# Performance work log

Measured on AMD Instinct MI355X. Metric: run time of the kernel, lower is better.

Reference implementation:

```python
import jax, jax.numpy as jnp
import numpy as np

B, T, H, W = 2, 8, 14, 14
S = H * W
DIM, HEADS = 768, 12
HD = DIM // HEADS  # 64


def setup_inputs() -> dict:
    key = jax.random.key(0)
    ks = jax.random.split(key, 6)
    std = 0.02
    return {
        "x": jax.random.normal(ks[0], (B, T, S, DIM), jnp.float32),
        "qkv_w": jax.random.normal(ks[1], (3 * DIM, DIM), jnp.float32) * std,
        "proj_w": jax.random.normal(ks[2], (DIM, DIM), jnp.float32) * std,
        "proj_b": jnp.zeros((DIM,), jnp.float32),
        "rel_pos_h": jax.random.normal(ks[3], (2 * H - 1, HD), jnp.float32) * std,
        "rel_pos_w": jax.random.normal(ks[4], (2 * W - 1, HD), jnp.float32) * std,
        "rel_pos_t": jax.random.normal(ks[5], (2 * T - 1, HD), jnp.float32) * std,
    }


def _rel_table(rel_pos, q_len):
    # q_len == k_len here, so get_rel_pos is identity and indices simplify
    idx = np.arange(q_len)[:, None] - np.arange(q_len)[None, :] + (q_len - 1)
    return rel_pos[idx]  # [q_len, k_len, head_dim]


def reference(x, qkv_w, proj_w, proj_b, rel_pos_h, rel_pos_w, rel_pos_t):
    B_, T_, S_, C = x.shape
    H_ = W_ = int(S_ ** 0.5)
    N = T_ * S_
    hd = C // HEADS
    scale = hd ** -0.5

    xf = x.reshape(B_, N, C)
    qkv = (xf @ qkv_w.T).reshape(B_, N, 3, HEADS, hd).transpose(2, 0, 3, 1, 4)
    q, k, v = qkv[0], qkv[1], qkv[2]  # each [B, heads, N, hd]

    attn = jnp.einsum('bhqd,bhkd->bhqk', q, k) * scale  # [B, heads, N, N]

    # Decomposed relative-position bias (note: uses UNscaled q, as in original)
    r_q = q.reshape(B_, HEADS, T_, H_, W_, hd)
    Rh = _rel_table(rel_pos_h, H_)  # [H, H, hd]
    Rw = _rel_table(rel_pos_w, W_)  # [W, W, hd]
    Rt = _rel_table(rel_pos_t, T_)  # [T, T, hd]
    rel_h = jnp.einsum('bythwc,hkc->bythwk', r_q, Rh)
    rel_w = jnp.einsum('bythwc,wkc->bythwk', r_q, Rw)
    rel_t = jnp.einsum('bythwc,tkc->bythwk', r_q, Rt)

    attn = (attn.reshape(B_, HEADS, T_, H_, W_, T_, H_, W_)
            + rel_h[:, :, :, :, :, None, :, None]
            + rel_w[:, :, :, :, :, None, None, :]
            + rel_t[:, :, :, :, :, :, None, None]
            ).reshape(B_, HEADS, N, N)

    attn = jax.nn.softmax(attn, axis=-1)
    out = jnp.einsum('bhqk,bhkd->bhqd', attn, v)  # [B, heads, N, hd]
    out = out.transpose(0, 2, 1, 3).reshape(B_, N, C)
    out = out @ proj_w.T + proj_b
    return out.reshape(B_, T_, S_, C)
```

## Files before the change

### kernel.cpp

```cpp
#include <hip/hip_runtime.h>

using f16   = _Float16;
using f16x4 = __attribute__((ext_vector_type(4))) _Float16;
using f16x8 = __attribute__((ext_vector_type(8))) _Float16;
using f32x4 = __attribute__((ext_vector_type(4))) float;
using u32x4 = __attribute__((ext_vector_type(4))) unsigned int;
using fp16x2_raw = __fp16 __attribute__((ext_vector_type(2)));

#define MFMA16(a, b, c) __builtin_amdgcn_mfma_f32_16x16x32_f16((a), (b), (c), 0, 0, 0)

namespace {
constexpr int kT = 8, kWd = 14, kS = 196;
constexpr int kN = 1568;
constexpr int kM = 3136;
constexpr int kHeads = 12;
constexpr int kNp = 1664;
constexpr float kLog2e = 1.4426950408889634f;
constexpr size_t OFF_WH   = 0;
constexpr size_t OFF_WP   = 3538944;
constexpr size_t OFF_Q    = 4718592;
constexpr size_t OFF_XH   = 9830400;
constexpr size_t OFF_KF   = 14942208;
constexpr size_t OFF_KONE = 20054016;
constexpr size_t OFF_VSWZ = 20267008;
constexpr size_t WS_TOTAL = 25378816;
constexpr int kKoneTot = 13 * 8 * 2 * 64 * 8;

__device__ inline f16x4 pack4(float4 v) {
  union { fp16x2_raw h2[2]; f16x4 f4; } u;
  u.h2[0] = __builtin_amdgcn_cvt_pkrtz(v.x, v.y);
  u.h2[1] = __builtin_amdgcn_cvt_pkrtz(v.z, v.w);
  return u.f4;
}

__device__ inline float fast_exp2(float x) {
#if __has_builtin(__builtin_amdgcn_exp2f)
  return __builtin_amdgcn_exp2f(x);
#else
  return __expf(x * 0.6931471805599453f);
#endif
}

__device__ inline void gload_lds16(const f16* g, f16* l) {
  __builtin_amdgcn_global_load_lds(
      (const __attribute__((address_space(1))) unsigned int*)g,
      (__attribute__((address_space(3))) unsigned int*)l,
      16, 0, 0);
}

__device__ inline float dotqLDS(const f16x8* qh, const f16* Rrow) {
  float s = 0.f;
#pragma unroll
  for (int i = 0; i < 8; ++i) {
    f16x8 a = qh[i];
    f16x8 b = *(const f16x8*)(Rrow + i * 8);
#pragma unroll
    for (int k = 0; k < 8; ++k) s += (float)a[k] * (float)b[k];
  }
  return s;
}
}

__global__ __launch_bounds__(256) void arp_cvt(
    const float* __restrict__ qkvw, const float* __restrict__ projw,
    const float* __restrict__ X,
    f16* __restrict__ Wh, f16* __restrict__ Wp, f16* __restrict__ Xh,
    f16* __restrict__ konefrag) {
  int gid = blockIdx.x * 256 + threadIdx.x;
  const int NQ = (2304 * 768) / 4;
  const int NP = (768 * 768) / 4;
  const int NX = (3136 * 768) / 4;
  if (gid < NQ) {
    *(f16x4*)(Wh + (size_t)gid * 4) = pack4(*(const float4*)(qkvw + (size_t)gid * 4));
  } else if (gid < NQ + NP) {
    int g = gid - NQ;
    *(f16x4*)(Wp + (size_t)g * 4) = pack4(*(const float4*)(projw + (size_t)g * 4));
  } else if (gid < NQ + NP + NX) {
    int g = gid - NQ - NP;
    *(f16x4*)(Xh + (size_t)g * 4) = pack4(*(const float4*)(X + (size_t)g * 4));
  } else {
    int g = gid - NQ - NP - NX;
    if (g < kKoneTot) {
      int j = g & 7;
      int lane = (g >> 3) & 63;
      int s2 = (g >> 9) & 1;
      int nt = (g >> 10) & 7;
      int kt = g >> 13;
      int slot = lane & 15, qd = lane >> 4;
      int kin = (nt >> 1) * 32 + (slot >> 2) * 8 + (nt & 1) * 4 + (slot & 3);
      int key = kt * 128 + kin;
      int c = s2 * 32 + qd * 8 + j;
      int t2 = key / kS; int rm = key - t2 * kS;
      int h2 = rm / kWd; int w2 = rm - h2 * kWd;
      if (t2 > kT - 1) t2 = kT - 1;
      float v = 0.f;
      if (c == h2) v = 1.f;
      else if (c == 14 + w2) v = 1.f;
      else if (c == 28 + t2) v = 1.f;
      else if (c == 36 && key >= kN) v = 1.f;
      konefrag[g] = (f16)v;
    }
  }
}

__global__ __launch_bounds__(256, 2) void arp_gemm_qkv(
    const f16* __restrict__ Xh, const f16* __restrict__ Wh,
    f16* __restrict__ qf, f16* __restrict__ kfrag, f16* __restrict__ vswz) {
  __shared__ char smem[34816];
  f16* sA = (f16*)smem;
  f16* sB = (f16*)(smem + 10240);
  f16* sE = (f16*)smem;
  const int tid = threadIdx.x, lane = tid & 63, wv = tid >> 6;
  const int m0 = blockIdx.y * 128, n0 = blockIdx.x * 128;
  const int wm = (wv & 1) * 64, wn = (wv >> 1) * 64;
  const int frow = lane & 15, quad = lane >> 4, fcol = quad * 8;
  const f32x4 vzero = {0.f, 0.f, 0.f, 0.f};
  f32x4 acc[4][4];
#pragma unroll
  for (int i = 0; i < 4; ++i)
#pragma unroll
    for (int j = 0; j < 4; ++j) acc[i][j] = vzero;

  u32x4 pA[2], pB[2];
  const u32x4 uz = {0, 0, 0, 0};
#pragma unroll
  for (int i = 0; i < 2; ++i) {
    int idx = i * 256 + tid;
    int r = idx >> 2, c8 = (idx & 3) * 8;
    int gm = m0 + r;
    pA[i] = (gm < kM) ? *(const u32x4*)(Xh + (size_t)gm * 768 + c8) : uz;
    pB[i] = *(const u32x4*)(Wh + (size_t)(n0 + r) * 768 + c8);
  }

  for (int kt = 0; kt < 24; ++kt) {
#pragma unroll
    for (int i = 0; i < 2; ++i) {
      int idx = i * 256 + tid;
      int r = idx >> 2, c8 = (idx & 3) * 8;
      *(u32x4*)&sA[r * 40 + c8] = pA[i];
      *(u32x4*)&sB[r * 40 + c8] = pB[i];
    }
    __syncthreads();
    if (kt < 23) {
      int ko = (kt + 1) * 32;
#pragma unroll
      for (int i = 0; i < 2; ++i) {
        int idx = i * 256 + tid;
        int r = idx >> 2, c8 = (idx & 3) * 8;
        int gm = m0 + r;
        pA[i] = (gm < kM) ? *(const u32x4*)(Xh + (size_t)gm * 768 + ko + c8) : uz;
        pB[i] = *(const u32x4*)(Wh + (size_t)(n0 + r) * 768 + ko + c8);
      }
    }
    f16x8 af[4], bf[4];
#pragma unroll
    for (int t = 0; t < 4; ++t) {
      af[t] = *(const f16x8*)&sA[(wm + t * 16 + frow) * 40 + fcol];
      bf[t] = *(const f16x8*)&sB[(wn + t * 16 + frow) * 40 + fcol];
    }
#pragma unroll
    for (int mt = 0; mt < 4; ++mt)
#pragma unroll
      for (int nt = 0; nt < 4; ++nt)
        acc[mt][nt] = MFMA16(af[mt], bf[nt], acc[mt][nt]);
    __syncthreads();
  }

  const int which = n0 / 768;
  if (which == 2) {
#pragma unroll
    for (int mt = 0; mt < 4; ++mt)
#pragma unroll
      for (int nt = 0; nt < 4; ++nt) {
        int cl = wn + nt * 16 + frow;
#pragma unroll
        for (int rg = 0; rg < 4; ++rg) {
          int rl = wm + mt * 16 + quad * 4 + rg;
          sE[cl * 136 + rl] = (f16)acc[mt][nt][rg];
        }
      }
    __syncthreads();
    int cl = tid >> 1;
    int rb = (tid & 1) * 64;
    int rem = n0 + cl - 1536;
    int hh = rem >> 6, d = rem & 63;
    int td = d >> 4, fr = d & 15;
#pragma unroll
    for (int j = 0; j < 8; ++j) {
      int ms = m0 + rb + j * 8;
      if (ms < kM) {
        int bb = (ms >= kN) ? 1 : 0;
        int ns = ms - bb * kN;
        int bh = bb * kHeads + hh;
        int kt2 = ns >> 7, kr = ns & 127;
        int kc = kr >> 5, qd = (kr >> 3) & 3;
        f16* dst = vswz + ((((size_t)(bh * 13 + kt2)) * 4 + td) * 4 + kc) * 512
                        + (qd * 16 + fr) * 8;
        *(u32x4*)dst = *(const u32x4*)&sE[cl * 136 + rb + j * 8];
      }
    }
  } else {
#pragma unroll
    for (int mt = 0; mt < 4; ++mt) {
      int rbase = m0 + wm + mt * 16 + quad * 4;
#pragma unroll
      for (int nt = 0; nt < 4; ++nt) {
        int col0 = n0 + wn + nt * 16;
        int rem = col0 - which * 768;
        int hh = rem >> 6;
        int d = (rem & 63) + frow;
        int s = d >> 5, qd2 = (d >> 3) & 3, j = d & 7;
#pragma unroll
        for (int rg = 0; rg < 4; ++rg) {
          int m = rbase + rg;
          if (m < kM) {
            int bb = (m >= kN) ? 1 : 0;
            int ns = m - bb * kN;
            int bh = bb * kHeads + hh;
            float av = acc[mt][nt][rg];
            if (which == 0) {
              av *= kLog2e;
              qf[((size_t)bh * kNp + ns) * 64 + d] = (f16)av;
            } else {
              av *= 0.125f;
              int kt2 = ns >> 7;
              int kin = ns & 127;
              int nt2 = ((kin >> 5) << 1) | ((kin >> 2) & 1);
              int slot = ((kin >> 3) & 3) * 4 + (kin & 3);
              kfrag[(((size_t)(bh * 13 + kt2) * 8 + nt2) * 2 + s) * 512
                    + (qd2 * 16 + slot) * 8 + j] = (f16)av;
            }
          }
        }
      }
    }
  }
}

__global__ __launch_bounds__(256, 3) void arp_attn(
    const f16* qf,
    const float* __restrict__ Rh, const float* __restrict__ Rw, const float* __restrict__ Rt,
    const f16* __restrict__ kfrag, const f16* __restrict__ konefrag,
    const f16* __restrict__ vswz, f16* qfO) {
  __shared__ char pool[49152];
  f16* sKa = (f16*)pool;
  f16* sKb = (f16*)(pool + 16384);
  f16* sV  = (f16*)(pool + 32768);
  f16* sQE = (f16*)pool;
  f16* sR  = (f16*)(pool + 8192);

  const int tid = threadIdx.x, lane = tid & 63, wv = tid >> 6;
  const int q0 = blockIdx.x * 64;
  const int bh = blockIdx.y;
  const int frow = lane & 15, quad = lane >> 4;
  const f32x4 vzero = {0.f, 0.f, 0.f, 0.f};

  const f16* kba = kfrag + (size_t)bh * 13 * 8192;
  const f16* vba = vswz + (size_t)bh * 13 * 8192;

  for (int g = tid; g < 69 * 16; g += 256) {
    int row = g >> 4, c4 = (g & 15) * 4;
    const float* src = (row < 27) ? Rh + row * 64 + c4
                     : (row < 54) ? Rw + (row - 27) * 64 + c4
                                  : Rt + (row - 54) * 64 + c4;
    *(f16x4*)&sR[row * 72 + c4] = pack4(*(const float4*)src);
  }
  __syncthreads();

  {
    int q = q0 + lane;
    int qc = (q < kN) ? q : kN - 1;
    int tq = qc / kS, sr = qc - tq * kS;
    int hq = sr / kWd, wq = sr - hq * kWd;
    if (wv < 3) {
      f16x8 qh[8];
      const f16x8* qv8 = (const f16x8*)(qf + ((size_t)bh * kNp + q) * 64);
#pragma unroll
      for (int i = 0; i < 8; ++i) qh[i] = qv8[i];
      if (wv == 0) {
#pragma unroll
        for (int e = 0; e < 14; ++e)
          sQE[lane * 64 + e] = (f16)dotqLDS(qh, &sR[(hq - e + 13) * 72]);
      } else if (wv == 1) {
#pragma unroll
        for (int e = 0; e < 14; ++e)
          sQE[lane * 64 + 14 + e] = (f16)dotqLDS(qh, &sR[(wq - e + 40) * 72]);
      } else {
#pragma unroll
        for (int e = 0; e < 8; ++e)
          sQE[lane * 64 + 28 + e] = (f16)dotqLDS(qh, &sR[(tq - e + 61) * 72]);
      }
    } else {
      sQE[lane * 64 + 36] = (f16)(-30000.f);
#pragma unroll
      for (int e = 37; e < 64; ++e) sQE[lane * 64 + e] = (f16)0.f;
    }
  }
  __syncthreads();

  f16x8 aQ0, aQ1, aQE0, aQE1;
  {
    int row = q0 + wv * 16 + frow;
    const f16* qp = qf + ((size_t)bh * kNp + row) * 64;
    aQ0 = *(const f16x8*)(qp + quad * 8);
    aQ1 = *(const f16x8*)(qp + 32 + quad * 8);
    int rl = wv * 16 + frow;
    aQE0 = *(const f16x8*)&sQE[rl * 64 + quad * 8];
    aQE1 = *(const f16x8*)&sQE[rl * 64 + 32 + quad * 8];
  }
  __syncthreads();

#pragma unroll
  for (int i = 0; i < 4; ++i) {
    int u = (i * 256 + tid) * 8;
    gload_lds16(kba + u, sKa + u);
    gload_lds16(konefrag + u, sKb + u);
    gload_lds16(vba + u, sV + u);
  }

  float den = 0.f;
  f32x4 Oc[4];
#pragma unroll
  for (int t = 0; t < 4; ++t) Oc[t] = vzero;

  for (int kt = 0; kt < 13; ++kt) {
    __syncthreads();

    f32x4 Sc[8];
    __builtin_amdgcn_s_setprio(1);
#pragma unroll
    for (int nt = 0; nt < 8; ++nt) {
      const f16* ka = &sKa[nt * 1024 + lane * 8];
      const f16* kb = &sKb[nt * 1024 + lane * 8];
      f32x4 s = MFMA16(*(const f16x8*)(ka), aQ0, vzero);
      s = MFMA16(*(const f16x8*)(ka + 512), aQ1, s);
      s = MFMA16(*(const f16x8*)(kb), aQE0, s);
      Sc[nt] = MFMA16(*(const f16x8*)(kb + 512), aQE1, s);
    }
    __builtin_amdgcn_s_setprio(0);
    f16x8 bV[4][4];
#pragma unroll
    for (int td = 0; td < 4; ++td)
#pragma unroll
      for (int kc = 0; kc < 4; ++kc)
        bV[td][kc] = *(const f16x8*)&sV[(td * 4 + kc) * 512 + lane * 8];
    __syncthreads();

    if (kt < 12) {
      const f16* kfa = kba + (size_t)(kt + 1) * 8192;
      const f16* koa = konefrag + (size_t)(kt + 1) * 8192;
      const f16* vfa = vba + (size_t)(kt + 1) * 8192;
#pragma unroll
      for (int i = 0; i < 4; ++i) {
        int u = (i * 256 + tid) * 8;
        gload_lds16(kfa + u, sKa + u);
        gload_lds16(koa + u, sKb + u);
        gload_lds16(vfa + u, sV + u);
      }
    }

#pragma unroll
    for (int nt = 0; nt < 8; ++nt)
#pragma unroll
      for (int r = 0; r < 4; ++r)
        Sc[nt][r] = fast_exp2(Sc[nt][r]);

    __builtin_amdgcn_s_setprio(1);
#pragma unroll
    for (int kc = 0; kc < 4; ++kc) {
      union { _Float16 h[8]; f16x8 v; } up;
#pragma unroll
      for (int r = 0; r < 4; ++r) {
        up.h[r]     = (f16)Sc[2 * kc][r];
        up.h[4 + r] = (f16)Sc[2 * kc + 1][r];
      }
#pragma unroll
      for (int r = 0; r < 4; ++r)
        den += (float)up.h[r] + (float)up.h[4 + r];
#pragma unroll
      for (int td = 0; td < 4; ++td)
        Oc[td] = MFMA16(up.v, bV[td][kc], Oc[td]);
    }
    __builtin_amdgcn_s_setprio(0);
  }

  den += __shfl_xor(den, 16, 64);
  den += __shfl_xor(den, 32, 64);
  float lr[4];
#pragma unroll
  for (int r = 0; r < 4; ++r)
    lr[r] = 1.f / __shfl(den, quad * 4 + r, 64);
#pragma unroll
  for (int td = 0; td < 4; ++td)
#pragma unroll
    for (int r = 0; r < 4; ++r) {
      int row = q0 + wv * 16 + quad * 4 + r;
      if (row < kN) {
        float val = Oc[td][r] * lr[r];
        qfO[((size_t)bh * kNp + row) * 64 + td * 16 + frow] = (f16)val;
      }
    }
}

__global__ __launch_bounds__(256, 4) void arp_gemm_proj(
    const f16* A, const f16* __restrict__ Wp,
    const float* __restrict__ bias, float* __restrict__ out) {
  __shared__ f16 sA[64 * 40];
  __shared__ f16 sB[128 * 40];
  const int tid = threadIdx.x, lane = tid & 63, wv = tid >> 6;
  const int m0 = blockIdx.y * 64, n0 = blockIdx.x * 128;
  const int frow = lane & 15, quad = lane >> 4, fcol = quad * 8;
  const f32x4 vzero = {0.f, 0.f, 0.f, 0.f};
  f32x4 acc[8];
#pragma unroll
  for (int j = 0; j < 8; ++j) acc[j] = vzero;

  u32x4 pA, pB[2];
  {
    int r = tid >> 2, c8 = (tid & 3) * 8;
    int m = m0 + r;
    int bb = (m >= kN) ? 1 : 0;
    int ns = m - bb * kN;
    pA = *(const u32x4*)(A + ((size_t)(bb * kHeads) * kNp + ns) * 64 + c8);
#pragma unroll
    for (int i = 0; i < 2; ++i) {
      int idx = i * 256 + tid;
      int rb2 = idx >> 2, cb8 = (idx & 3) * 8;
      pB[i] = *(const u32x4*)(Wp + (size_t)(n0 + rb2) * 768 + cb8);
    }
  }

  for (int kt = 0; kt < 24; ++kt) {
    {
      int r = tid >> 2, c8 = (tid & 3) * 8;
      *(u32x4*)&sA[r * 40 + c8] = pA;
#pragma unroll
      for (int i = 0; i < 2; ++i) {
        int idx = i * 256 + tid;
        int rb2 = idx >> 2, cb8 = (idx & 3) * 8;
        *(u32x4*)&sB[rb2 * 40 + cb8] = pB[i];
      }
    }
    __syncthreads();
    if (kt < 23) {
      int k1 = kt + 1;
      int hd = k1 >> 1, dof = (k1 & 1) * 32;
      int r = tid >> 2, c8 = (tid & 3) * 8;
      int m = m0 + r;
      int bb = (m >= kN) ? 1 : 0;
      int ns = m - bb * kN;
      pA = *(const u32x4*)(A + ((size_t)(bb * kHeads + hd) * kNp + ns) * 64 + dof + c8);
#pragma unroll
      for (int i = 0; i < 2; ++i) {
        int idx = i * 256 + tid;
        int rb2 = idx >> 2, cb8 = (idx & 3) * 8;
        pB[i] = *(const u32x4*)(Wp + (size_t)(n0 + rb2) * 768 + k1 * 32 + cb8);
      }
    }
    f16x8 af = *(const f16x8*)&sA[(wv * 16 + frow) * 40 + fcol];
    f16x8 bf[8];
#pragma unroll
    for (int u = 0; u < 8; ++u)
      bf[u] = *(const f16x8*)&sB[(u * 16 + frow) * 40 + fcol];
#pragma unroll
    for (int u = 0; u < 8; ++u)
      acc[u] = MFMA16(af, bf[u], acc[u]);
    __syncthreads();
  }
#pragma unroll
  for (int u = 0; u < 8; ++u) {
    int col = n0 + u * 16 + frow;
    float bv = bias[col];
#pragma unroll
    for (int rg = 0; rg < 4; ++rg) {
      int m = m0 + wv * 16 + quad * 4 + rg;
      out[(size_t)m * 768 + col] = acc[u][rg] + bv;
    }
  }
}

extern "C" void kernel_launch(void* const* d_in, const int* in_sizes, int n_in,
                              void* d_out, int out_size, void* d_ws, size_t ws_size,
                              hipStream_t stream) {
  if (ws_size < WS_TOTAL) return;
  const float* x      = (const float*)d_in[0];
  const float* qkv_w  = (const float*)d_in[1];
  const float* proj_w = (const float*)d_in[2];
  const float* proj_b = (const float*)d_in[3];
  const float* rph    = (const float*)d_in[4];
  const float* rpw    = (const float*)d_in[5];
  const float* rpt    = (const float*)d_in[6];
  char* ws = (char*)d_ws;
  f16* Wh       = (f16*)(ws + OFF_WH);
  f16* Wp       = (f16*)(ws + OFF_WP);
  f16* qf       = (f16*)(ws + OFF_Q);
  f16* Xh       = (f16*)(ws + OFF_XH);
  f16* kfrag    = (f16*)(ws + OFF_KF);
  f16* konefrag = (f16*)(ws + OFF_KONE);
  f16* vswz     = (f16*)(ws + OFF_VSWZ);

  const int cvtTot = (2304 * 768 + 768 * 768 + 3136 * 768) / 4 + kKoneTot;
  arp_cvt<<<(cvtTot + 255) / 256, 256, 0, stream>>>(qkv_w, proj_w, x, Wh, Wp, Xh, konefrag);
  arp_gemm_qkv<<<dim3(18, 25), 256, 0, stream>>>(Xh, Wh, qf, kfrag, vswz);
  arp_attn<<<dim3(25, 24), 256, 0, stream>>>(qf, rph, rpw, rpt, kfrag, konefrag, vswz, qf);
  arp_gemm_proj<<<dim3(6, 49), 256, 0, stream>>>(qf, Wp, proj_b, (float*)d_out);
}
```

Before: 173.0 us.

## Split attention key tiles across two wave groups with LDS reduction

The attention block grows from 256 to 512 threads. Each pair of waves shares a 16-row query fragment, and each wave handles half of the 128 keys in every key tile. The partial outputs and denominators from the second half are summed through shared memory at the end. This doubles the waves available per block to hide latency and halves per-wave register use. The cost is an extra LDS reduction and synchronisation, and possibly fewer resident blocks per CU.

```diff
diff --git a/kernel.cpp b/kernel.cpp
--- a/kernel.cpp
+++ b/kernel.cpp
@@ -237,7 +237,7 @@
   }
 }
 
-__global__ __launch_bounds__(256, 3) void arp_attn(
+__global__ __launch_bounds__(512, 6) void arp_attn(
     const f16* qf,
     const float* __restrict__ Rh, const float* __restrict__ Rw, const float* __restrict__ Rt,
     const f16* __restrict__ kfrag, const f16* __restrict__ konefrag,
@@ -253,12 +253,14 @@
   const int q0 = blockIdx.x * 64;
   const int bh = blockIdx.y;
   const int frow = lane & 15, quad = lane >> 4;
+  const int rf = wv & 3;
+  const int kh = wv >> 2;
   const f32x4 vzero = {0.f, 0.f, 0.f, 0.f};
 
   const f16* kba = kfrag + (size_t)bh * 13 * 8192;
   const f16* vba = vswz + (size_t)bh * 13 * 8192;
 
-  for (int g = tid; g < 69 * 16; g += 256) {
+  for (int g = tid; g < 69 * 16; g += 512) {
     int row = g >> 4, c4 = (g & 15) * 4;
     const float* src = (row < 27) ? Rh + row * 64 + c4
                      : (row < 54) ? Rw + (row - 27) * 64 + c4
@@ -290,7 +292,7 @@
         for (int e = 0; e < 8; ++e)
           sQE[lane * 64 + 28 + e] = (f16)dotqLDS(qh, &sR[(tq - e + 61) * 72]);
       }
-    } else {
+    } else if (wv == 3) {
       sQE[lane * 64 + 36] = (f16)(-30000.f);
 #pragma unroll
       for (int e = 37; e < 64; ++e) sQE[lane * 64 + e] = (f16)0.f;
@@ -300,22 +302,21 @@
 
   f16x8 aQ0, aQ1, aQE0, aQE1;
   {
-    int row = q0 + wv * 16 + frow;
+    int row = q0 + rf * 16 + frow;
     const f16* qp = qf + ((size_t)bh * kNp + row) * 64;
     aQ0 = *(const f16x8*)(qp + quad * 8);
     aQ1 = *(const f16x8*)(qp + 32 + quad * 8);
-    int rl = wv * 16 + frow;
+    int rl = rf * 16 + frow;
     aQE0 = *(const f16x8*)&sQE[rl * 64 + quad * 8];
     aQE1 = *(const f16x8*)&sQE[rl * 64 + 32 + quad * 8];
   }
   __syncthreads();
 
-#pragma unroll
-  for (int i = 0; i < 4; ++i) {
-    int u = (i * 256 + tid) * 8;
-    gload_lds16(kba + u, sKa + u);
-    gload_lds16(konefrag + u, sKb + u);
-    gload_lds16(vba + u, sV + u);
+  {
+    int u0 = tid * 8, u1 = (512 + tid) * 8;
+    gload_lds16(kba + u0, sKa + u0);      gload_lds16(kba + u1, sKa + u1);
+    gload_lds16(konefrag + u0, sKb + u0); gload_lds16(konefrag + u1, sKb + u1);
+    gload_lds16(vba + u0, sV + u0);       gload_lds16(vba + u1, sV + u1);
   }
 
   float den = 0.f;
@@ -323,83 +324,104 @@
 #pragma unroll
   for (int t = 0; t < 4; ++t) Oc[t] = vzero;
 
+  const int nth = kh * 4;
+  const int kcb = kh * 2;
+
   for (int kt = 0; kt < 13; ++kt) {
     __syncthreads();
 
-    f32x4 Sc[8];
+    f32x4 Sc[4];
     __builtin_amdgcn_s_setprio(1);
 #pragma unroll
-    for (int nt = 0; nt < 8; ++nt) {
-      const f16* ka = &sKa[nt * 1024 + lane * 8];
-      const f16* kb = &sKb[nt * 1024 + lane * 8];
+    for (int nt2 = 0; nt2 < 4; ++nt2) {
+      const f16* ka = &sKa[(nth + nt2) * 1024 + lane * 8];
+      const f16* kb = &sKb[(nth + nt2) * 1024 + lane * 8];
       f32x4 s = MFMA16(*(const f16x8*)(ka), aQ0, vzero);
       s = MFMA16(*(const f16x8*)(ka + 512), aQ1, s);
       s = MFMA16(*(const f16x8*)(kb), aQE0, s);
-      Sc[nt] = MFMA16(*(const f16x8*)(kb + 512), aQE1, s);
+      Sc[nt2] = MFMA16(*(const f16x8*)(kb + 512), aQE1, s);
     }
     __builtin_amdgcn_s_setprio(0);
-    f16x8 bV[4][4];
+    f16x8 bV[4][2];
 #pragma unroll
     for (int td = 0; td < 4; ++td)
 #pragma unroll
-      for (int kc = 0; kc < 4; ++kc)
-        bV[td][kc] = *(const f16x8*)&sV[(td * 4 + kc) * 512 + lane * 8];
+      for (int kcl = 0; kcl < 2; ++kcl)
+        bV[td][kcl] = *(const f16x8*)&sV[(td * 4 + kcb + kcl) * 512 + lane * 8];
     __syncthreads();
 
     if (kt < 12) {
       const f16* kfa = kba + (size_t)(kt + 1) * 8192;
       const f16* koa = konefrag + (size_t)(kt + 1) * 8192;
       const f16* vfa = vba + (size_t)(kt + 1) * 8192;
-#pragma unroll
-      for (int i = 0; i < 4; ++i) {
-        int u = (i * 256 + tid) * 8;
-        gload_lds16(kfa + u, sKa + u);
-        gload_lds16(koa + u, sKb + u);
-        gload_lds16(vfa + u, sV + u);
-      }
-    }
-
-#pragma unroll
-    for (int nt = 0; nt < 8; ++nt)
+      int u0 = tid * 8, u1 = (512 + tid) * 8;
+      gload_lds16(kfa + u0, sKa + u0); gload_lds16(kfa + u1, sKa + u1);
+      gload_lds16(koa + u0, sKb + u0); gload_lds16(koa + u1, sKb + u1);
+      gload_lds16(vfa + u0, sV + u0);  gload_lds16(vfa + u1, sV + u1);
+    }
+
+#pragma unroll
+    for (int nt2 = 0; nt2 < 4; ++nt2)
 #pragma unroll
       for (int r = 0; r < 4; ++r)
-        Sc[nt][r] = fast_exp2(Sc[nt][r]);
+        Sc[nt2][r] = fast_exp2(Sc[nt2][r]);
 
     __builtin_amdgcn_s_setprio(1);
 #pragma unroll
-    for (int kc = 0; kc < 4; ++kc) {
+    for (int kcl = 0; kcl < 2; ++kcl) {
       union { _Float16 h[8]; f16x8 v; } up;
 #pragma unroll
       for (int r = 0; r < 4; ++r) {
-        up.h[r]     = (f16)Sc[2 * kc][r];
-        up.h[4 + r] = (f16)Sc[2 * kc + 1][r];
+        up.h[r]     = (f16)Sc[2 * kcl][r];
+        up.h[4 + r] = (f16)Sc[2 * kcl + 1][r];
       }
 #pragma unroll
       for (int r = 0; r < 4; ++r)
         den += (float)up.h[r] + (float)up.h[4 + r];
 #pragma unroll
       for (int td = 0; td < 4; ++td)
-        Oc[td] = MFMA16(up.v, bV[td][kc], Oc[td]);
+        Oc[td] = MFMA16(up.v, bV[td][kcl], Oc[td]);
     }
     __builtin_amdgcn_s_setprio(0);
   }
 
   den += __shfl_xor(den, 16, 64);
   den += __shfl_xor(den, 32, 64);
-  float lr[4];
-#pragma unroll
-  for (int r = 0; r < 4; ++r)
-    lr[r] = 1.f / __shfl(den, quad * 4 + r, 64);
-#pragma unroll
-  for (int td = 0; td < 4; ++td)
-#pragma unroll
-    for (int r = 0; r < 4; ++r) {
-      int row = q0 + wv * 16 + quad * 4 + r;
-      if (row < kN) {
-        float val = Oc[td][r] * lr[r];
-        qfO[((size_t)bh * kNp + row) * 64 + td * 16 + frow] = (f16)val;
-      }
-    }
+
+  __syncthreads();
+  float* sOc  = (float*)pool;
+  float* sDen = (float*)(pool + 16384);
+  if (kh == 1) {
+    if (quad == 0) sDen[rf * 16 + frow] = den;
+#pragma unroll
+    for (int td = 0; td < 4; ++td)
+#pragma unroll
+      for (int r = 0; r < 4; ++r)
+        sOc[rf * 1024 + (quad * 4 + r) * 64 + td * 16 + frow] = Oc[td][r];
+  }
+  __syncthreads();
+  if (kh == 0) {
+    den += sDen[rf * 16 + frow];
+#pragma unroll
+    for (int td = 0; td < 4; ++td)
+#pragma unroll
+      for (int r = 0; r < 4; ++r)
+        Oc[td][r] += sOc[rf * 1024 + (quad * 4 + r) * 64 + td * 16 + frow];
+    float lr[4];
+#pragma unroll
+    for (int r = 0; r < 4; ++r)
+      lr[r] = 1.f / __shfl(den, quad * 4 + r, 64);
+#pragma unroll
+    for (int td = 0; td < 4; ++td)
+#pragma unroll
+      for (int r = 0; r < 4; ++r) {
+        int row = q0 + rf * 16 + quad * 4 + r;
+        if (row < kN) {
+          float val = Oc[td][r] * lr[r];
+          qfO[((size_t)bh * kNp + row) * 64 + td * 16 + frow] = (f16)val;
+        }
+      }
+  }
 }
 
 __global__ __launch_bounds__(256, 4) void arp_gemm_proj(
@@ -502,6 +524,6 @@
   const int cvtTot = (2304 * 768 + 768 * 768 + 3136 * 768) / 4 + kKoneTot;
   arp_cvt<<<(cvtTot + 255) / 256, 256, 0, stream>>>(qkv_w, proj_w, x, Wh, Wp, Xh, konefrag);
   arp_gemm_qkv<<<dim3(18, 25), 256, 0, stream>>>(Xh, Wh, qf, kfrag, vswz);
-  arp_attn<<<dim3(25, 24), 256, 0, stream>>>(qf, rph, rpw, rpt, kfrag, konefrag, vswz, qf);
+  arp_attn<<<dim3(25, 24), 512, 0, stream>>>(qf, rph, rpw, rpt, kfrag, konefrag, vswz, qf);
   arp_gemm_proj<<<dim3(6, 49), 256, 0, stream>>>(qf, Wp, proj_b, (float*)d_out);
 }
```

After: 229.4 us. 32.6% more time.
